# Kernel tuning notes

Measured on AMD Instinct MI355X. Metric: run time of the kernel, lower is better.

## Reference

```python
import jax, jax.numpy as jnp
import numpy as np

IN_CH = 128
INTER = max(IN_CH // 8, 1)  # 16

def setup_inputs() -> dict:
    key = jax.random.key(0)
    ks = jax.random.split(key, 10)
    B, C, D, H, W = 2, IN_CH, 16, 24, 24
    s = 1.0 / np.sqrt(C)
    so = 1.0 / np.sqrt(INTER)
    return {
        "x":  jax.random.normal(ks[0], (B, C, D, H, W), dtype=jnp.float32),
        "Wq": jax.random.normal(ks[1], (INTER, C), dtype=jnp.float32) * s,
        "bq": jax.random.normal(ks[2], (INTER,), dtype=jnp.float32) * 0.01,
        "Wk": jax.random.normal(ks[3], (INTER, C), dtype=jnp.float32) * s,
        "bk": jax.random.normal(ks[4], (INTER,), dtype=jnp.float32) * 0.01,
        "Wv": jax.random.normal(ks[5], (INTER, C), dtype=jnp.float32) * s,
        "bv": jax.random.normal(ks[6], (INTER,), dtype=jnp.float32) * 0.01,
        "Wo": jax.random.normal(ks[7], (C, INTER), dtype=jnp.float32) * so,
        "bo": jax.random.normal(ks[8], (C,), dtype=jnp.float32) * 0.01,
        "gamma": jnp.zeros((1,), dtype=jnp.float32) + 0.5,  # nonzero so attn path is exercised
    }

def reference(x, Wq, bq, Wk, bk, Wv, bv, Wo, bo, gamma):
    B, C, D, H, W = x.shape
    N = D * H * W
    xf = x.reshape(B, C, N)  # flatten spatial
    # 1x1x1 conv == per-voxel channel matmul
    q = jnp.einsum('ic,bcn->bin', Wq, xf) + bq[None, :, None]  # [B,I,N]
    k = jnp.einsum('ic,bcn->bin', Wk, xf) + bk[None, :, None]
    v = jnp.einsum('ic,bcn->bin', Wv, xf) + bv[None, :, None]
    # attention[b,n,m] = sum_i q[b,i,n] k[b,i,m]; softmax over keys m
    attn = jax.nn.softmax(jnp.einsum('bin,bim->bnm', q, k), axis=-1)
    # out[b,c,n] = sum_m v[b,c,m] attn[b,n,m]
    out = jnp.einsum('bim,bnm->bin', v, attn)  # [B,I,N]
    out = jnp.einsum('ci,bin->bcn', Wo, out) + bo[None, :, None]
    out = out.reshape(B, C, D, H, W)
    return gamma[0] * out + x
```

## Files before the change

### kernel.cpp

```cpp
#include <hip/hip_runtime.h>

#define C_CH 128
#define I_CH 16
#define NVOX 9216
#define BATCH 2
#define NGRP (NVOX / 32)
#define LOG2E 1.44269504088896340736f

typedef unsigned short ushort_t;
typedef unsigned int uint_t;
typedef short bf16x4 __attribute__((ext_vector_type(4)));
typedef short bf16x8 __attribute__((ext_vector_type(8)));
typedef float f32x4 __attribute__((ext_vector_type(4)));

static __device__ inline ushort_t f2bf_rne(float x) {
    uint_t u = __builtin_bit_cast(uint_t, x);
    u = (u + 0x7FFFu + ((u >> 16) & 1u)) >> 16;
    return (ushort_t)u;
}

static __device__ inline float fast_exp2(float x) {
#if __has_builtin(__builtin_amdgcn_exp2f)
    return __builtin_amdgcn_exp2f(x);
#else
    return exp2f(x);
#endif
}

static __device__ inline f32x4 score_mfma(bf16x4 a, bf16x4 b, f32x4 c) {
#if __has_builtin(__builtin_amdgcn_mfma_f32_16x16x16bf16_1k)
    return __builtin_amdgcn_mfma_f32_16x16x16bf16_1k(a, b, c, 0, 0, 0);
#elif __has_builtin(__builtin_amdgcn_mfma_f32_16x16x16_bf16)
    return __builtin_amdgcn_mfma_f32_16x16x16_bf16(a, b, c, 0, 0, 0);
#else
    int2 ai = __builtin_bit_cast(int2, a);
    int2 bi = __builtin_bit_cast(int2, b);
    int4 a4 = make_int4(ai.x, ai.y, 0, 0);
    int4 b4 = make_int4(bi.x, bi.y, 0, 0);
    return __builtin_amdgcn_mfma_f32_16x16x32_bf16(
        __builtin_bit_cast(bf16x8, a4), __builtin_bit_cast(bf16x8, b4), c, 0, 0, 0);
#endif
}

__global__ __launch_bounds__(256) void qkv_kernel(
    const float* __restrict__ x,
    const float* __restrict__ Wq, const float* __restrict__ bq,
    const float* __restrict__ Wk, const float* __restrict__ bk,
    const float* __restrict__ Wv, const float* __restrict__ bv,
    ushort_t* __restrict__ qb, ushort_t* __restrict__ kfrag,
    ushort_t* __restrict__ vfrag)
{
    __shared__ float ws[3][I_CH][132];
    __shared__ float xs[C_CH][I_CH];

    const int t    = threadIdx.x;
    const int vox0 = blockIdx.x * 16;
    const int b    = vox0 / NVOX;
    const int n0   = vox0 - b * NVOX;

    {
        const int i  = t >> 4;
        const int c8 = (t & 15) * 8;
        const float4* wq4 = (const float4*)(Wq + i * C_CH + c8);
        const float4* wk4 = (const float4*)(Wk + i * C_CH + c8);
        const float4* wv4 = (const float4*)(Wv + i * C_CH + c8);
        *(float4*)&ws[0][i][c8]     = wq4[0];
        *(float4*)&ws[0][i][c8 + 4] = wq4[1];
        *(float4*)&ws[1][i][c8]     = wk4[0];
        *(float4*)&ws[1][i][c8 + 4] = wk4[1];
        *(float4*)&ws[2][i][c8]     = wv4[0];
        *(float4*)&ws[2][i][c8 + 4] = wv4[1];
    }

    {
        const float* xb = x + (size_t)b * C_CH * NVOX + n0;
        const int c   = t >> 2;
        const int col = (t & 3) * 4;
        *(float4*)&xs[c][col]      = *(const float4*)(xb + (size_t)c * NVOX + col);
        *(float4*)&xs[c + 64][col] = *(const float4*)(xb + (size_t)(c + 64) * NVOX + col);
    }
    __syncthreads();

    const int n = t & 15;
    const int i = t >> 4;

    float aq = 0.f, ak = 0.f, av = 0.f;
    #pragma unroll 4
    for (int c = 0; c < C_CH; c += 4) {
        float x0 = xs[c + 0][n];
        float x1 = xs[c + 1][n];
        float x2 = xs[c + 2][n];
        float x3 = xs[c + 3][n];
        float4 wq = *(const float4*)&ws[0][i][c];
        float4 wk = *(const float4*)&ws[1][i][c];
        float4 wv = *(const float4*)&ws[2][i][c];
        aq = fmaf(wq.x, x0, fmaf(wq.y, x1, fmaf(wq.z, x2, fmaf(wq.w, x3, aq))));
        ak = fmaf(wk.x, x0, fmaf(wk.y, x1, fmaf(wk.z, x2, fmaf(wk.w, x3, ak))));
        av = fmaf(wv.x, x0, fmaf(wv.y, x1, fmaf(wv.z, x2, fmaf(wv.w, x3, av))));
    }

    const int nl     = n0 + n;
    const size_t vox = (size_t)b * NVOX + nl;
    qb[vox * I_CH + i] = f2bf_rne((aq + bq[i]) * LOG2E);

    const int g   = nl >> 5;
    const int k32 = nl & 31;
    const size_t gbase = ((size_t)b * NGRP + g) * 512;

    {
        const int tile = (k32 >> 2) & 1;
        const int m    = k32 - 4 * tile;
        const int l16  = ((m >> 3) << 2) | (m & 3);
        const int lane = ((i >> 2) << 4) | l16;
        kfrag[gbase + tile * 256 + lane * 4 + (i & 3)] = f2bf_rne(ak + bk[i]);
    }
    {
        const int lane = ((k32 >> 3) << 4) | i;
        vfrag[gbase + lane * 8 + (k32 & 7)] = f2bf_rne(av + bv[i]);
    }
}

__global__ __launch_bounds__(512) void attn_kernel(
    const ushort_t* __restrict__ qb, const ushort_t* __restrict__ kfrag,
    const ushort_t* __restrict__ vfrag,
    const float* __restrict__ Wo, const float* __restrict__ bo,
    const float* __restrict__ gamma, const float* __restrict__ x,
    float* __restrict__ out)
{
    __shared__ float po[4][32][18];
    __shared__ float lsh[8][33];
    __shared__ float aot[16][40];
    __shared__ float wo_s[C_CH][17];

    const int tid  = threadIdx.x;
    const int w    = tid >> 6;
    const int lane = tid & 63;
    const int l16  = lane & 15;
    const int quad = lane >> 4;

    {
        const int c  = tid >> 2;
        const int i4 = (tid & 3) * 4;
        float4 wv = *(const float4*)(Wo + c * I_CH + i4);
        wo_s[c][i4 + 0] = wv.x; wo_s[c][i4 + 1] = wv.y;
        wo_s[c][i4 + 2] = wv.z; wo_s[c][i4 + 3] = wv.w;
    }

    const int qvox0 = blockIdx.x * 32;
    const int b     = qvox0 / NVOX;
    const int nloc0 = qvox0 - b * NVOX;

    bf16x4 qf0 = __builtin_bit_cast(bf16x4,
        *(const int2*)(qb + (size_t)(qvox0 + l16) * I_CH + quad * 4));
    bf16x4 qf1 = __builtin_bit_cast(bf16x4,
        *(const int2*)(qb + (size_t)(qvox0 + 16 + l16) * I_CH + quad * 4));

    const ushort_t* kp = kfrag + ((size_t)b * NGRP + w * 36) * 512 + lane * 4;
    const ushort_t* vp = vfrag + ((size_t)b * NGRP + w * 36) * 512 + lane * 8;

    f32x4 O0 = {0.f,0.f,0.f,0.f}, O1 = {0.f,0.f,0.f,0.f};
    f32x4 L0 = {0.f,0.f,0.f,0.f}, L1 = {0.f,0.f,0.f,0.f};
    const f32x4 Z = {0.f,0.f,0.f,0.f};
    int4 onesi; onesi.x = onesi.y = onesi.z = onesi.w = 0x3F803F80;
    const bf16x8 ones = __builtin_bit_cast(bf16x8, onesi);

    int2 ka0 = *(const int2*)(kp);
    int2 ka1 = *(const int2*)(kp + 256);
    int4 va  = *(const int4*)(vp);

    #pragma unroll 2
    for (int it = 0; it < 36; ++it) {
        kp += 512;
        vp += 512;
        int2 ka0n = *(const int2*)(kp);
        int2 ka1n = *(const int2*)(kp + 256);
        int4 van  = *(const int4*)(vp);

        bf16x4 kA0 = __builtin_bit_cast(bf16x4, ka0);
        bf16x4 kA1 = __builtin_bit_cast(bf16x4, ka1);
        f32x4 s00 = score_mfma(kA0, qf0, Z);
        f32x4 s01 = score_mfma(kA1, qf0, Z);
        f32x4 s10 = score_mfma(kA0, qf1, Z);
        f32x4 s11 = score_mfma(kA1, qf1, Z);

        {
            float p00 = fast_exp2(s00.x), p01 = fast_exp2(s00.y);
            float p02 = fast_exp2(s00.z), p03 = fast_exp2(s00.w);
            float p10 = fast_exp2(s01.x), p11 = fast_exp2(s01.y);
            float p12 = fast_exp2(s01.z), p13 = fast_exp2(s01.w);
            uint_t d0 = __builtin_amdgcn_perm(__builtin_bit_cast(uint_t, p01),
                                              __builtin_bit_cast(uint_t, p00), 0x07060302u);
            uint_t d1 = __builtin_amdgcn_perm(__builtin_bit_cast(uint_t, p03),
                                              __builtin_bit_cast(uint_t, p02), 0x07060302u);
            uint_t d2 = __builtin_amdgcn_perm(__builtin_bit_cast(uint_t, p11),
                                              __builtin_bit_cast(uint_t, p10), 0x07060302u);
            uint_t d3 = __builtin_amdgcn_perm(__builtin_bit_cast(uint_t, p13),
                                              __builtin_bit_cast(uint_t, p12), 0x07060302u);
            int4 pbi = make_int4((int)d0, (int)d1, (int)d2, (int)d3);
            bf16x8 pb = __builtin_bit_cast(bf16x8, pbi);
            O0 = __builtin_amdgcn_mfma_f32_16x16x32_bf16(
                __builtin_bit_cast(bf16x8, va), pb, O0, 0, 0, 0);
            L0 = __builtin_amdgcn_mfma_f32_16x16x32_bf16(ones, pb, L0, 0, 0, 0);
        }
        {
            float p00 = fast_exp2(s10.x), p01 = fast_exp2(s10.y);
            float p02 = fast_exp2(s10.z), p03 = fast_exp2(s10.w);
            float p10 = fast_exp2(s11.x), p11 = fast_exp2(s11.y);
            float p12 = fast_exp2(s11.z), p13 = fast_exp2(s11.w);
            uint_t d0 = __builtin_amdgcn_perm(__builtin_bit_cast(uint_t, p01),
                                              __builtin_bit_cast(uint_t, p00), 0x07060302u);
            uint_t d1 = __builtin_amdgcn_perm(__builtin_bit_cast(uint_t, p03),
                                              __builtin_bit_cast(uint_t, p02), 0x07060302u);
            uint_t d2 = __builtin_amdgcn_perm(__builtin_bit_cast(uint_t, p11),
                                              __builtin_bit_cast(uint_t, p10), 0x07060302u);
            uint_t d3 = __builtin_amdgcn_perm(__builtin_bit_cast(uint_t, p13),
                                              __builtin_bit_cast(uint_t, p12), 0x07060302u);
            int4 pbi = make_int4((int)d0, (int)d1, (int)d2, (int)d3);
            bf16x8 pb = __builtin_bit_cast(bf16x8, pbi);
            O1 = __builtin_amdgcn_mfma_f32_16x16x32_bf16(
                __builtin_bit_cast(bf16x8, va), pb, O1, 0, 0, 0);
            L1 = __builtin_amdgcn_mfma_f32_16x16x32_bf16(ones, pb, L1, 0, 0, 0);
        }

        ka0 = ka0n; ka1 = ka1n; va = van;
    }

    if (w < 4) {
        #pragma unroll
        for (int r = 0; r < 4; ++r) {
            po[w][quad * 4 + r][l16]      = O0[r];
            po[w][16 + quad * 4 + r][l16] = O1[r];
        }
    }
    if (quad == 0) { lsh[w][l16] = L0.x; lsh[w][16 + l16] = L1.x; }
    __syncthreads();

    if (w >= 4) {
        #pragma unroll
        for (int r = 0; r < 4; ++r) {
            po[w - 4][quad * 4 + r][l16]      += O0[r];
            po[w - 4][16 + quad * 4 + r][l16] += O1[r];
        }
    }
    __syncthreads();

    {
        const int q32 = tid & 31;
        const int i   = tid >> 5;
        const int row = (q32 >> 4) * 16 + i;
        const int col = q32 & 15;
        float v = 0.f, l = 0.f;
        #pragma unroll
        for (int ww = 0; ww < 4; ++ww) v += po[ww][row][col];
        #pragma unroll
        for (int ww = 0; ww < 8; ++ww) l += lsh[ww][q32];
        aot[i][q32] = v / l;
    }
    __syncthreads();

    const float g  = gamma[0];
    const int   c  = tid >> 2;
    const int   qh = (tid & 3) * 8;

    float acc[8];
    {
        const float b0 = bo[c];
        #pragma unroll
        for (int q = 0; q < 8; ++q) acc[q] = b0;
    }
    #pragma unroll
    for (int i = 0; i < 16; ++i) {
        const float wv = wo_s[c][i];
        float4 a0 = *(const float4*)&aot[i][qh];
        float4 a1 = *(const float4*)&aot[i][qh + 4];
        acc[0] = fmaf(wv, a0.x, acc[0]); acc[1] = fmaf(wv, a0.y, acc[1]);
        acc[2] = fmaf(wv, a0.z, acc[2]); acc[3] = fmaf(wv, a0.w, acc[3]);
        acc[4] = fmaf(wv, a1.x, acc[4]); acc[5] = fmaf(wv, a1.y, acc[5]);
        acc[6] = fmaf(wv, a1.z, acc[6]); acc[7] = fmaf(wv, a1.w, acc[7]);
    }

    const size_t gi = ((size_t)b * C_CH + c) * NVOX + nloc0 + qh;
    float4 x0 = *(const float4*)(x + gi);
    float4 x1 = *(const float4*)(x + gi + 4);
    float4 o0, o1;
    o0.x = fmaf(g, acc[0], x0.x); o0.y = fmaf(g, acc[1], x0.y);
    o0.z = fmaf(g, acc[2], x0.z); o0.w = fmaf(g, acc[3], x0.w);
    o1.x = fmaf(g, acc[4], x1.x); o1.y = fmaf(g, acc[5], x1.y);
    o1.z = fmaf(g, acc[6], x1.z); o1.w = fmaf(g, acc[7], x1.w);
    *(float4*)(out + gi)     = o0;
    *(float4*)(out + gi + 4) = o1;
}

extern "C" void kernel_launch(void* const* d_in, const int* in_sizes, int n_in,
                              void* d_out, int out_size, void* d_ws, size_t ws_size,
                              hipStream_t stream) {
    const float* x     = (const float*)d_in[0];
    const float* Wq    = (const float*)d_in[1];
    const float* bq    = (const float*)d_in[2];
    const float* Wk    = (const float*)d_in[3];
    const float* bk    = (const float*)d_in[4];
    const float* Wv    = (const float*)d_in[5];
    const float* bv    = (const float*)d_in[6];
    const float* Wo    = (const float*)d_in[7];
    const float* bo    = (const float*)d_in[8];
    const float* gamma = (const float*)d_in[9];
    float* out = (float*)d_out;

    ushort_t* qb    = (ushort_t*)d_ws;
    ushort_t* kfrag = qb    + (size_t)BATCH * NVOX * I_CH;
    ushort_t* vfrag = kfrag + (size_t)BATCH * NGRP * 512;

    hipLaunchKernelGGL(qkv_kernel, dim3(BATCH * NVOX / 16), dim3(256), 0, stream,
                       x, Wq, bq, Wk, bk, Wv, bv, qb, kfrag, vfrag);
    hipLaunchKernelGGL(attn_kernel, dim3(BATCH * NVOX / 32), dim3(512), 0, stream,
                       qb, kfrag, vfrag, Wo, bo, gamma, x, out);
}
```

Baseline: 114.3 us.

## Interleave K fragments for 16-byte loads, prefetch two iterations, use packed bf16 convert

Stores each lane's two K tiles next to each other so the attention loop fetches K with a single 128-bit load instead of two 64-bit loads. The K/V software pipeline now prefetches two iterations ahead rather than one, to hide more global-memory latency. P is packed to bf16 with the hardware packed-convert instruction when available; this rounds where the old byte permute truncated. The deeper prefetch adds registers, and the prefetch can read past the last group of each wave's range.

```diff
diff --git a/kernel.cpp b/kernel.cpp
--- a/kernel.cpp
+++ b/kernel.cpp
@@ -24,6 +24,15 @@
     return __builtin_amdgcn_exp2f(x);
 #else
     return exp2f(x);
+#endif
+}
+
+static __device__ inline uint_t pack_bf16(float a, float b) {
+#if __has_builtin(__builtin_amdgcn_cvt_pk_bf16_f32)
+    return __builtin_bit_cast(uint_t, __builtin_amdgcn_cvt_pk_bf16_f32(a, b));
+#else
+    return __builtin_amdgcn_perm(__builtin_bit_cast(uint_t, b),
+                                 __builtin_bit_cast(uint_t, a), 0x07060302u);
 #endif
 }
 
@@ -112,7 +121,7 @@
         const int m    = k32 - 4 * tile;
         const int l16  = ((m >> 3) << 2) | (m & 3);
         const int lane = ((i >> 2) << 4) | l16;
-        kfrag[gbase + tile * 256 + lane * 4 + (i & 3)] = f2bf_rne(ak + bk[i]);
+        kfrag[gbase + lane * 8 + tile * 4 + (i & 3)] = f2bf_rne(ak + bk[i]);
     }
     {
         const int lane = ((k32 >> 3) << 4) | i;
@@ -155,7 +164,7 @@
     bf16x4 qf1 = __builtin_bit_cast(bf16x4,
         *(const int2*)(qb + (size_t)(qvox0 + 16 + l16) * I_CH + quad * 4));
 
-    const ushort_t* kp = kfrag + ((size_t)b * NGRP + w * 36) * 512 + lane * 4;
+    const ushort_t* kp = kfrag + ((size_t)b * NGRP + w * 36) * 512 + lane * 8;
     const ushort_t* vp = vfrag + ((size_t)b * NGRP + w * 36) * 512 + lane * 8;
 
     f32x4 O0 = {0.f,0.f,0.f,0.f}, O1 = {0.f,0.f,0.f,0.f};
@@ -164,20 +173,20 @@
     int4 onesi; onesi.x = onesi.y = onesi.z = onesi.w = 0x3F803F80;
     const bf16x8 ones = __builtin_bit_cast(bf16x8, onesi);
 
-    int2 ka0 = *(const int2*)(kp);
-    int2 ka1 = *(const int2*)(kp + 256);
-    int4 va  = *(const int4*)(vp);
+    int4 k0 = *(const int4*)(kp);
+    int4 v0 = *(const int4*)(vp);
+    int4 k1 = *(const int4*)(kp + 512);
+    int4 v1 = *(const int4*)(vp + 512);
+    kp += 1024; vp += 1024;
 
     #pragma unroll 2
     for (int it = 0; it < 36; ++it) {
-        kp += 512;
-        vp += 512;
-        int2 ka0n = *(const int2*)(kp);
-        int2 ka1n = *(const int2*)(kp + 256);
-        int4 van  = *(const int4*)(vp);
-
-        bf16x4 kA0 = __builtin_bit_cast(bf16x4, ka0);
-        bf16x4 kA1 = __builtin_bit_cast(bf16x4, ka1);
+        int4 kn = *(const int4*)(kp);
+        int4 vn = *(const int4*)(vp);
+        kp += 512; vp += 512;
+
+        bf16x4 kA0 = __builtin_bit_cast(bf16x4, make_int2(k0.x, k0.y));
+        bf16x4 kA1 = __builtin_bit_cast(bf16x4, make_int2(k0.z, k0.w));
         f32x4 s00 = score_mfma(kA0, qf0, Z);
         f32x4 s01 = score_mfma(kA1, qf0, Z);
         f32x4 s10 = score_mfma(kA0, qf1, Z);
@@ -188,18 +197,11 @@
             float p02 = fast_exp2(s00.z), p03 = fast_exp2(s00.w);
             float p10 = fast_exp2(s01.x), p11 = fast_exp2(s01.y);
             float p12 = fast_exp2(s01.z), p13 = fast_exp2(s01.w);
-            uint_t d0 = __builtin_amdgcn_perm(__builtin_bit_cast(uint_t, p01),
-                                              __builtin_bit_cast(uint_t, p00), 0x07060302u);
-            uint_t d1 = __builtin_amdgcn_perm(__builtin_bit_cast(uint_t, p03),
-                                              __builtin_bit_cast(uint_t, p02), 0x07060302u);
-            uint_t d2 = __builtin_amdgcn_perm(__builtin_bit_cast(uint_t, p11),
-                                              __builtin_bit_cast(uint_t, p10), 0x07060302u);
-            uint_t d3 = __builtin_amdgcn_perm(__builtin_bit_cast(uint_t, p13),
-                                              __builtin_bit_cast(uint_t, p12), 0x07060302u);
-            int4 pbi = make_int4((int)d0, (int)d1, (int)d2, (int)d3);
+            int4 pbi = make_int4((int)pack_bf16(p00, p01), (int)pack_bf16(p02, p03),
+                                 (int)pack_bf16(p10, p11), (int)pack_bf16(p12, p13));
             bf16x8 pb = __builtin_bit_cast(bf16x8, pbi);
             O0 = __builtin_amdgcn_mfma_f32_16x16x32_bf16(
-                __builtin_bit_cast(bf16x8, va), pb, O0, 0, 0, 0);
+                __builtin_bit_cast(bf16x8, v0), pb, O0, 0, 0, 0);
             L0 = __builtin_amdgcn_mfma_f32_16x16x32_bf16(ones, pb, L0, 0, 0, 0);
         }
         {
@@ -207,22 +209,15 @@
             float p02 = fast_exp2(s10.z), p03 = fast_exp2(s10.w);
             float p10 = fast_exp2(s11.x), p11 = fast_exp2(s11.y);
             float p12 = fast_exp2(s11.z), p13 = fast_exp2(s11.w);
-            uint_t d0 = __builtin_amdgcn_perm(__builtin_bit_cast(uint_t, p01),
-                                              __builtin_bit_cast(uint_t, p00), 0x07060302u);
-            uint_t d1 = __builtin_amdgcn_perm(__builtin_bit_cast(uint_t, p03),
-                                              __builtin_bit_cast(uint_t, p02), 0x07060302u);
-            uint_t d2 = __builtin_amdgcn_perm(__builtin_bit_cast(uint_t, p11),
-                                              __builtin_bit_cast(uint_t, p10), 0x07060302u);
-            uint_t d3 = __builtin_amdgcn_perm(__builtin_bit_cast(uint_t, p13),
-                                              __builtin_bit_cast(uint_t, p12), 0x07060302u);
-            int4 pbi = make_int4((int)d0, (int)d1, (int)d2, (int)d3);
+            int4 pbi = make_int4((int)pack_bf16(p00, p01), (int)pack_bf16(p02, p03),
+                                 (int)pack_bf16(p10, p11), (int)pack_bf16(p12, p13));
             bf16x8 pb = __builtin_bit_cast(bf16x8, pbi);
             O1 = __builtin_amdgcn_mfma_f32_16x16x32_bf16(
-                __builtin_bit_cast(bf16x8, va), pb, O1, 0, 0, 0);
+                __builtin_bit_cast(bf16x8, v0), pb, O1, 0, 0, 0);
             L1 = __builtin_amdgcn_mfma_f32_16x16x32_bf16(ones, pb, L1, 0, 0, 0);
         }
 
-        ka0 = ka0n; ka1 = ka1n; va = van;
+        k0 = k1; v0 = v1; k1 = kn; v1 = vn;
     }
 
     if (w < 4) {
```

Result: no change. 116.1 us (+1.6%).
